# Kernel tuning notes

Hardware: AMD Instinct MI355X
Metric: run time of the kernel (lower is better)

The kernel has to match this reference:

```python
import jax, jax.numpy as jnp
import numpy as np

N_NODES = 25000
N_EDGES = 400000
N_GRAPHS = 1000
HID = 185
IN_CH = 9
EPS = 1e-5  # BatchNorm eps (eval mode: uses running stats)


def setup_inputs() -> dict:
    key = jax.random.key(0)
    ks = jax.random.split(key, 12)
    x = jax.random.normal(ks[0], (N_NODES, IN_CH), jnp.float32)
    edge_index = jax.random.randint(ks[1], (2, N_EDGES), 0, N_NODES, jnp.int32)
    batch = jnp.sort(jax.random.randint(ks[2], (N_NODES,), 0, N_GRAPHS, jnp.int32))
    W0 = jax.random.normal(ks[3], (IN_CH, HID), jnp.float32) * 0.3
    b0 = jnp.zeros((HID,), jnp.float32)
    W_h = jax.random.normal(ks[4], (3, HID, HID), jnp.float32) * 0.07
    b_h = jnp.zeros((3, HID), jnp.float32)
    bn_gamma = 1.0 + 0.1 * jax.random.normal(ks[5], (4, HID), jnp.float32)
    bn_beta = 0.1 * jax.random.normal(ks[6], (4, HID), jnp.float32)
    bn_mean = 0.1 * jax.random.normal(ks[7], (4, HID), jnp.float32)
    bn_var = jax.random.uniform(ks[8], (4, HID), jnp.float32, 0.5, 1.5)
    W_jk = jax.random.normal(ks[9], (4 * HID, HID), jnp.float32) * 0.05
    b_jk = jnp.zeros((HID,), jnp.float32)
    W_out = jax.random.normal(ks[10], (HID, 1), jnp.float32) * 0.1
    b_out = jnp.zeros((1,), jnp.float32)
    return dict(x=x, edge_index=edge_index, batch=batch, W0=W0, b0=b0,
                W_h=W_h, b_h=b_h, bn_gamma=bn_gamma, bn_beta=bn_beta,
                bn_mean=bn_mean, bn_var=bn_var, W_jk=W_jk, b_jk=b_jk,
                W_out=W_out, b_out=b_out)


def reference(x, edge_index, batch, W0, b0, W_h, b_h, bn_gamma, bn_beta,
              bn_mean, bn_var, W_jk, b_jk, W_out, b_out):
    N = x.shape[0]
    # GCN normalization with self-loops (gcn_norm, edge_weight = 1)
    loop = jnp.arange(N, dtype=edge_index.dtype)
    src = jnp.concatenate([edge_index[0], loop])  # [E+N]
    dst = jnp.concatenate([edge_index[1], loop])  # [E+N]
    deg = jax.ops.segment_sum(jnp.ones_like(dst, dtype=x.dtype), dst, num_segments=N)
    dis = jnp.where(deg > 0, jax.lax.rsqrt(jnp.maximum(deg, 1.0)), 0.0)
    enorm = dis[src] * dis[dst]  # [E+N]

    def gcn_conv(h, W, b):
        h = h @ W                                   # [N, HID]
        msg = h[src] * enorm[:, None]               # gather + scale, [E+N, HID]
        return jax.ops.segment_sum(msg, dst, num_segments=N) + b

    def bn_relu(h, i):
        h = (h - bn_mean[i]) * jax.lax.rsqrt(bn_var[i] + EPS) * bn_gamma[i] + bn_beta[i]
        return jax.nn.relu(h)  # dropout is identity in eval mode

    xs = []
    h = bn_relu(gcn_conv(x, W0, b0), 0)
    xs.append(h)
    for i in range(3):
        h = bn_relu(gcn_conv(h, W_h[i], b_h[i]), i + 1)
        xs.append(h)
    # JumpingKnowledge 'cat' + internal lin (740 -> 185)
    h = jnp.concatenate(xs, axis=-1) @ W_jk + b_jk  # [N, HID]
    # global_max_pool over graphs
    pooled = jax.ops.segment_max(h, batch, num_segments=N_GRAPHS)  # [G, HID]
    return pooled @ W_out + b_out  # [G, 1]
```

## Files before the change

kernel.cpp:

```cpp
#include <hip/hip_runtime.h>
#include <hip/hip_bf16.h>

#define N_NODES 25000
#define N_EDGES 400000
#define N_GRAPHS 1000
#define HID 185
#define EPS 1e-5f
#define XPITCH 768

typedef __attribute__((ext_vector_type(8))) short bf16x8;
typedef __attribute__((ext_vector_type(4))) float f32x4;

__device__ __forceinline__ short f2bf(float f) {
    union { float f; unsigned u; } v; v.f = f;
    unsigned r = v.u + 0x7FFFu + ((v.u >> 16) & 1u);
    return (short)(r >> 16);
}
__device__ __forceinline__ float bfl(unsigned u) { return __uint_as_float(u << 16); }
__device__ __forceinline__ float bfh(unsigned u) { return __uint_as_float(u & 0xFFFF0000u); }
__device__ __forceinline__ unsigned pk2(float lo, float hi) {
    return (unsigned)(unsigned short)f2bf(lo) | ((unsigned)(unsigned short)f2bf(hi) << 16);
}

#define GLD16(g, l) __builtin_amdgcn_global_load_lds( \
    (const __attribute__((address_space(1))) unsigned*)(const void*)(g), \
    (__attribute__((address_space(3))) unsigned*)(void*)(l), 16, 0, 0)

__global__ void k_init(int* cnt, int* cursor) {
    int i = blockIdx.x * blockDim.x + threadIdx.x;
    if (i < N_NODES) { cnt[i] = 0; cursor[i] = 0; }
}

__global__ void k_deg(const int* __restrict__ dst, int* cnt, int E) {
    int i = blockIdx.x * blockDim.x + threadIdx.x;
    if (i < E) atomicAdd(&cnt[dst[i]], 1);
}

__global__ __launch_bounds__(256) void k_scan_part(const int* __restrict__ cnt,
                                                   int* __restrict__ bsum,
                                                   float* __restrict__ dis, int N) {
    int i = blockIdx.x * 256 + threadIdx.x;
    int v = (i < N) ? cnt[i] : 0;
    if (i < N) dis[i] = rsqrtf((float)(v + 1));
    #pragma unroll
    for (int off = 32; off; off >>= 1) v += __shfl_down(v, off);
    __shared__ int s[4];
    if ((threadIdx.x & 63) == 0) s[threadIdx.x >> 6] = v;
    __syncthreads();
    if (threadIdx.x == 0) bsum[blockIdx.x] = s[0] + s[1] + s[2] + s[3];
}

__global__ __launch_bounds__(128) void k_scan_mid(const int* __restrict__ bsum,
                                                  int* __restrict__ boff, int NB) {
    __shared__ int s[128];
    int t = threadIdx.x;
    int v = (t < NB) ? bsum[t] : 0;
    s[t] = v; __syncthreads();
    for (int off = 1; off < 128; off <<= 1) {
        int x = (t >= off) ? s[t - off] : 0;
        __syncthreads();
        s[t] += x;
        __syncthreads();
    }
    if (t < NB) boff[t] = s[t] - v;
}

__global__ __launch_bounds__(256) void k_scan_add(const int* __restrict__ cnt,
                                                  const int* __restrict__ boff,
                                                  int* __restrict__ rowptr, int N) {
    __shared__ int s[256];
    int t = threadIdx.x;
    int i = blockIdx.x * 256 + t;
    int v = (i < N) ? cnt[i] : 0;
    s[t] = v; __syncthreads();
    for (int off = 1; off < 256; off <<= 1) {
        int x = (t >= off) ? s[t - off] : 0;
        __syncthreads();
        s[t] += x;
        __syncthreads();
    }
    if (i < N) rowptr[i + 1] = boff[blockIdx.x] + s[t];
    if (i == 0) rowptr[0] = 0;
}

__global__ void k_scatter(const int* __restrict__ src, const int* __restrict__ dst,
                          const float* __restrict__ dis, const int* __restrict__ rowptr,
                          int* cursor, int* __restrict__ csr_src,
                          float* __restrict__ csr_w, int E) {
    int e = blockIdx.x * blockDim.x + threadIdx.x;
    if (e < E) {
        int d = dst[e];
        int s = src[e];
        int pos = atomicAdd(&cursor[d], 1);
        int o = rowptr[d] + pos;
        csr_src[o] = s;
        csr_w[o] = dis[s];
    }
}

__global__ void k_prep_w(const float* __restrict__ W_h, const float* __restrict__ W_jk,
                         const float* __restrict__ b0, const float* __restrict__ b_h,
                         const float* __restrict__ gamma, const float* __restrict__ beta,
                         const float* __restrict__ mean, const float* __restrict__ var,
                         short* __restrict__ Wt_h, short* __restrict__ Wt_jk,
                         float* __restrict__ bnsc, float* __restrict__ bnsh) {
    int idx = blockIdx.x * 256 + threadIdx.x;
    const int HW = 3 * 192 * 192;
    const int JW = 192 * 768;
    if (idx < HW) {
        int l = idx / (192 * 192);
        int r = idx % (192 * 192);
        int n = r / 192, k = r % 192;
        float v = (n < HID && k < HID) ? W_h[(l * HID + k) * HID + n] : 0.0f;
        Wt_h[idx] = f2bf(v);
    } else if (idx < HW + JW) {
        int j2 = idx - HW;
        int n = j2 / 768, kk = j2 % 768;
        int l = kk / 192, j = kk % 192;
        float v = (n < HID && j < HID) ? W_jk[(l * HID + j) * HID + n] : 0.0f;
        Wt_jk[j2] = f2bf(v);
    } else if (idx < HW + JW + 4 * 192) {
        int li = idx - HW - JW;
        int l = li / 192, c = li % 192;
        float sc = 0.0f, sh = 0.0f;
        if (c < HID) {
            float bb = (l == 0) ? b0[c] : b_h[(l - 1) * HID + c];
            sc = rsqrtf(var[l * HID + c] + EPS) * gamma[l * HID + c];
            sh = (bb - mean[l * HID + c]) * sc + beta[l * HID + c];
        }
        bnsc[li] = sc;
        bnsh[li] = sh;
    }
}

__global__ void k_aggr0(const float* __restrict__ x, const float* __restrict__ dis,
                        const int* __restrict__ rowptr, const int* __restrict__ csr_src,
                        const float* __restrict__ csr_w, float* __restrict__ xa, int N) {
    int idx = blockIdx.x * blockDim.x + threadIdx.x;
    int n = idx >> 4;
    int c = idx & 15;
    if (n >= N || c >= 9) return;
    float dn = dis[n];
    float acc = x[n * 9 + c] * dn;
    int e = rowptr[n], end = rowptr[n + 1];
    for (; e + 4 <= end; e += 4) {
        int s0 = csr_src[e], s1 = csr_src[e + 1], s2 = csr_src[e + 2], s3 = csr_src[e + 3];
        float w0 = csr_w[e], w1 = csr_w[e + 1], w2 = csr_w[e + 2], w3 = csr_w[e + 3];
        float v0 = x[s0 * 9 + c], v1 = x[s1 * 9 + c], v2 = x[s2 * 9 + c], v3 = x[s3 * 9 + c];
        acc += v0 * w0 + v1 * w1 + v2 * w2 + v3 * w3;
    }
    for (; e < end; ++e)
        acc += x[csr_src[e] * 9 + c] * csr_w[e];
    xa[n * 9 + c] = acc * dn;
}

__global__ __launch_bounds__(192) void k_gemm0(const float* __restrict__ A,
                                               const float* __restrict__ W,
                                               const float* __restrict__ bnsc,
                                               const float* __restrict__ bnsh,
                                               short* __restrict__ xcat, int N) {
    __shared__ float As[8 * 9];
    const int tid = threadIdx.x;
    const int r0 = blockIdx.x * 8;
    for (int idx = tid; idx < 72; idx += 192) {
        int r = idx & 7, k = idx >> 3;
        int row = r0 + r;
        As[idx] = (row < N) ? A[row * 9 + k] : 0.0f;
    }
    __syncthreads();
    const int c = tid;
    float res[8];
    #pragma unroll
    for (int r = 0; r < 8; ++r) res[r] = 0.0f;
    if (c < HID) {
        float acc[8] = {0,0,0,0,0,0,0,0};
        for (int k = 0; k < 9; ++k) {
            float w = W[k * HID + c];
            #pragma unroll
            for (int r = 0; r < 8; ++r) acc[r] += As[k * 8 + r] * w;
        }
        float sc = bnsc[c], sh = bnsh[c];
        #pragma unroll
        for (int r = 0; r < 8; ++r)
            res[r] = fmaxf(acc[r] * sc + sh, 0.0f);
    }
    #pragma unroll
    for (int r = 0; r < 8; ++r) {
        int row = r0 + r;
        if (row < N) xcat[row * XPITCH + c] = (c < HID) ? f2bf(res[r]) : (short)0;
    }
}

template<int KCH>
__global__ __launch_bounds__(256, 3) void k_mgemm(const short* __restrict__ A,
                                                  const short* __restrict__ Bt,
                                                  short* __restrict__ Cout, int N) {
    __shared__ short As[2][64 * 32];
    const int tid = threadIdx.x;
    const int wave = tid >> 6;
    const int lane = tid & 63;
    const int quad = lane >> 4;
    const int lm = lane & 15;
    const int r0 = blockIdx.x * 64;
    const int KTOT = KCH * 32;
    const int srow = tid >> 2;
    const int sseg = (tid & 3) ^ ((srow >> 1) & 3);
    const long gbase = (long)(r0 + srow) * XPITCH + sseg * 8;
    const int axor = (lm >> 1) & 3;

    f32x4 acc[4][3];
    #pragma unroll
    for (int i = 0; i < 4; ++i)
        #pragma unroll
        for (int j = 0; j < 3; ++j) acc[i][j] = (f32x4){0.f, 0.f, 0.f, 0.f};

    GLD16(A + gbase, &As[0][tid * 8]);

    #pragma unroll
    for (int g = 0; g < KCH / 6; ++g) {
        bf16x8 b[3][6];
        #pragma unroll
        for (int j = 0; j < 6; ++j)
            #pragma unroll
            for (int nt = 0; nt < 3; ++nt)
                b[nt][j] = *(const bf16x8*)(Bt + (wave * 48 + nt * 16 + lm) * KTOT
                                            + (g * 6 + j) * 32 + quad * 8);
        #pragma unroll
        for (int j = 0; j < 6; ++j) {
            const int kc = g * 6 + j;
            __syncthreads();
            if (kc + 1 < KCH)
                GLD16(A + gbase + (kc + 1) * 32, &As[(kc + 1) & 1][tid * 8]);
            bf16x8 a[4];
            #pragma unroll
            for (int mt = 0; mt < 4; ++mt)
                a[mt] = *(const bf16x8*)(&As[kc & 1][(mt * 16 + lm) * 32 + (quad ^ axor) * 8]);
            #pragma unroll
            for (int mt = 0; mt < 4; ++mt)
                #pragma unroll
                for (int nt = 0; nt < 3; ++nt)
                    acc[mt][nt] = __builtin_amdgcn_mfma_f32_16x16x32_bf16(
                        a[mt], b[nt][j], acc[mt][nt], 0, 0, 0);
        }
    }
    #pragma unroll
    for (int mt = 0; mt < 4; ++mt) {
        #pragma unroll
        for (int nt = 0; nt < 3; ++nt) {
            int col = wave * 48 + nt * 16 + lm;
            #pragma unroll
            for (int r = 0; r < 4; ++r) {
                int row = r0 + mt * 16 + quad * 4 + r;
                if (row < N) Cout[row * 192 + col] = f2bf(acc[mt][nt][r]);
            }
        }
    }
}

__global__ __launch_bounds__(256) void k_aggr_bn(const short* __restrict__ tmp16,
                                                 const float* __restrict__ dis,
                                                 const int* __restrict__ rowptr,
                                                 const int* __restrict__ csr_src,
                                                 const float* __restrict__ csr_w,
                                                 const float* __restrict__ bnsc,
                                                 const float* __restrict__ bnsh,
                                                 short* __restrict__ outp, int N) {
    int n = (blockIdx.x << 2) + (threadIdx.x >> 6);
    if (n >= N) return;
    int lane = threadIdx.x & 63;
    int c0 = (lane < 48) ? (lane << 2) : 0;
    float dn = dis[n];
    float a0, a1, a2, a3;
    {
        uint2 v = *(const uint2*)(tmp16 + (size_t)n * 192 + c0);
        a0 = bfl(v.x) * dn; a1 = bfh(v.x) * dn; a2 = bfl(v.y) * dn; a3 = bfh(v.y) * dn;
    }
    int e = rowptr[n], end = rowptr[n + 1];
    for (; e + 4 <= end; e += 4) {
        int s0 = csr_src[e], s1 = csr_src[e + 1], s2 = csr_src[e + 2], s3 = csr_src[e + 3];
        float w0 = csr_w[e], w1 = csr_w[e + 1], w2 = csr_w[e + 2], w3 = csr_w[e + 3];
        uint2 v0 = *(const uint2*)(tmp16 + (size_t)s0 * 192 + c0);
        uint2 v1 = *(const uint2*)(tmp16 + (size_t)s1 * 192 + c0);
        uint2 v2 = *(const uint2*)(tmp16 + (size_t)s2 * 192 + c0);
        uint2 v3 = *(const uint2*)(tmp16 + (size_t)s3 * 192 + c0);
        a0 += bfl(v0.x) * w0; a1 += bfh(v0.x) * w0; a2 += bfl(v0.y) * w0; a3 += bfh(v0.y) * w0;
        a0 += bfl(v1.x) * w1; a1 += bfh(v1.x) * w1; a2 += bfl(v1.y) * w1; a3 += bfh(v1.y) * w1;
        a0 += bfl(v2.x) * w2; a1 += bfh(v2.x) * w2; a2 += bfl(v2.y) * w2; a3 += bfh(v2.y) * w2;
        a0 += bfl(v3.x) * w3; a1 += bfh(v3.x) * w3; a2 += bfl(v3.y) * w3; a3 += bfh(v3.y) * w3;
    }
    for (; e < end; ++e) {
        int s = csr_src[e];
        float w = csr_w[e];
        uint2 v = *(const uint2*)(tmp16 + (size_t)s * 192 + c0);
        a0 += bfl(v.x) * w; a1 += bfh(v.x) * w; a2 += bfl(v.y) * w; a3 += bfh(v.y) * w;
    }
    float4 sc = *(const float4*)(bnsc + c0);
    float4 sh = *(const float4*)(bnsh + c0);
    float o0 = fmaxf(a0 * dn * sc.x + sh.x, 0.0f);
    float o1 = fmaxf(a1 * dn * sc.y + sh.y, 0.0f);
    float o2 = fmaxf(a2 * dn * sc.z + sh.z, 0.0f);
    float o3 = fmaxf(a3 * dn * sc.w + sh.w, 0.0f);
    if (lane < 48) {
        uint2 p;
        p.x = pk2(o0, o1);
        p.y = pk2(o2, o3);
        *(uint2*)(outp + (size_t)n * XPITCH + c0) = p;
    }
}

__global__ __launch_bounds__(192) void k_pool_out(const short* __restrict__ jk,
                                                  const int* __restrict__ batch,
                                                  const float* __restrict__ b_jk,
                                                  const float* __restrict__ W_out,
                                                  const float* __restrict__ b_out,
                                                  float* __restrict__ out, int N) {
    __shared__ int bounds[2];
    __shared__ float partial[3];
    const int g = blockIdx.x;
    const int tid = threadIdx.x;
    if (tid < 2) {
        int key = g + tid;
        int lo = 0, hi = N;
        while (lo < hi) {
            int mid = (lo + hi) >> 1;
            if (batch[mid] < key) lo = mid + 1; else hi = mid;
        }
        bounds[tid] = lo;
    }
    __syncthreads();
    const int beg = bounds[0], end = bounds[1];
    float mx = -3.4e38f;
    for (int n = beg; n < end; ++n)
        mx = fmaxf(mx, bfl((unsigned)(unsigned short)jk[(size_t)n * 192 + tid]));
    float p = (tid < HID) ? (mx + b_jk[tid]) * W_out[tid] : 0.0f;
    #pragma unroll
    for (int off = 32; off; off >>= 1) p += __shfl_down(p, off);
    if ((tid & 63) == 0) partial[tid >> 6] = p;
    __syncthreads();
    if (tid == 0) out[g] = partial[0] + partial[1] + partial[2] + b_out[0];
}

extern "C" void kernel_launch(void* const* d_in, const int* in_sizes, int n_in,
                              void* d_out, int out_size, void* d_ws, size_t ws_size,
                              hipStream_t stream) {
    const float* x      = (const float*)d_in[0];
    const int*   ei     = (const int*)  d_in[1];
    const int*   batch  = (const int*)  d_in[2];
    const float* W0     = (const float*)d_in[3];
    const float* b0     = (const float*)d_in[4];
    const float* W_h    = (const float*)d_in[5];
    const float* b_h    = (const float*)d_in[6];
    const float* gamma  = (const float*)d_in[7];
    const float* beta   = (const float*)d_in[8];
    const float* mean   = (const float*)d_in[9];
    const float* var    = (const float*)d_in[10];
    const float* W_jk   = (const float*)d_in[11];
    const float* b_jk   = (const float*)d_in[12];
    const float* W_out  = (const float*)d_in[13];
    const float* b_out  = (const float*)d_in[14];
    float* out = (float*)d_out;

    const int N = N_NODES, E = N_EDGES, G = N_GRAPHS, H = HID;
    const int NB = (N + 255) / 256;

    float* dis   = (float*)d_ws;
    float* xa    = dis + 25024;
    float* csr_w = xa + 225024;
    float* bnsc  = csr_w + 400000;
    float* bnsh  = bnsc + 768;
    short* xcat  = (short*)(bnsh + 768);
    short* tmp16 = xcat + 19200000;
    short* Wt_h  = tmp16 + 4800000;
    short* Wt_jk = Wt_h + 110592;
    int* rowptr  = (int*)(Wt_jk + 147456);
    int* cnt     = rowptr + 25024;
    int* cursor  = cnt + 25024;
    int* csr_src = cursor + 25024;
    int* bsum    = csr_src + 400000;
    int* boff    = bsum + 128;

    const int* src = ei;
    const int* dst = ei + E;

    k_init<<<NB, 256, 0, stream>>>(cnt, cursor);
    k_deg<<<(E + 255) / 256, 256, 0, stream>>>(dst, cnt, E);
    k_scan_part<<<NB, 256, 0, stream>>>(cnt, bsum, dis, N);
    k_scan_mid<<<1, 128, 0, stream>>>(bsum, boff, NB);
    k_scan_add<<<NB, 256, 0, stream>>>(cnt, boff, rowptr, N);
    k_scatter<<<(E + 255) / 256, 256, 0, stream>>>(src, dst, dis, rowptr, cursor,
                                                   csr_src, csr_w, E);
    k_prep_w<<<(3 * 192 * 192 + 192 * 768 + 4 * 192 + 255) / 256, 256, 0, stream>>>(
        W_h, W_jk, b0, b_h, gamma, beta, mean, var, Wt_h, Wt_jk, bnsc, bnsh);

    k_aggr0<<<(N * 16 + 255) / 256, 256, 0, stream>>>(x, dis, rowptr, csr_src, csr_w, xa, N);
    k_gemm0<<<(N + 7) / 8, 192, 0, stream>>>(xa, W0, bnsc, bnsh, xcat, N);

    const int MB = (N + 63) / 64;
    for (int l = 1; l < 4; ++l) {
        k_mgemm<6><<<MB, 256, 0, stream>>>(xcat + (l - 1) * 192,
                                           Wt_h + (l - 1) * 192 * 192, tmp16, N);
        k_aggr_bn<<<(N + 3) / 4, 256, 0, stream>>>(tmp16, dis, rowptr, csr_src, csr_w,
                                                   bnsc + l * 192, bnsh + l * 192,
                                                   xcat + l * 192, N);
    }

    k_mgemm<24><<<MB, 256, 0, stream>>>(xcat, Wt_jk, tmp16, N);

    k_pool_out<<<G, 192, 0, stream>>>(tmp16, batch, b_jk, W_out, b_out, out, N);
}
```

Before: 317.3 us.

## Cut launches: merge setup, fold scan, fuse layer-0 aggregation into GEMM, drop LDS staging

Merges the count-zeroing and weight-prep kernels into one, removes the mid-scan kernel by having each block reduce preceding block sums itself, and reuses rowptr as the scatter cursor, which turns rowptr into end offsets. Layer-0 aggregation is fused into the small input GEMM, so the xa intermediate disappears. The MFMA GEMM loses its LDS double-buffered async loads and its occupancy hint, and now reads A and B fragments straight from global memory. This trades fewer launches and less LDS synchronization for GEMM loads that may be less efficient and more redundant.

```diff
diff --git a/kernel.cpp b/kernel.cpp
--- a/kernel.cpp
+++ b/kernel.cpp
@@ -22,13 +22,43 @@
     return (unsigned)(unsigned short)f2bf(lo) | ((unsigned)(unsigned short)f2bf(hi) << 16);
 }
 
-#define GLD16(g, l) __builtin_amdgcn_global_load_lds( \
-    (const __attribute__((address_space(1))) unsigned*)(const void*)(g), \
-    (__attribute__((address_space(3))) unsigned*)(void*)(l), 16, 0, 0)
-
-__global__ void k_init(int* cnt, int* cursor) {
-    int i = blockIdx.x * blockDim.x + threadIdx.x;
-    if (i < N_NODES) { cnt[i] = 0; cursor[i] = 0; }
+#define HW (3 * 192 * 192)
+#define JW (192 * 768)
+#define CNTPAD 25024
+__global__ void k_setup(const float* __restrict__ W_h, const float* __restrict__ W_jk,
+                        const float* __restrict__ b0, const float* __restrict__ b_h,
+                        const float* __restrict__ gamma, const float* __restrict__ beta,
+                        const float* __restrict__ mean, const float* __restrict__ var,
+                        int* __restrict__ cnt,
+                        short* __restrict__ Wt_h, short* __restrict__ Wt_jk,
+                        float* __restrict__ bnsc, float* __restrict__ bnsh) {
+    int idx = blockIdx.x * 256 + threadIdx.x;
+    if (idx < CNTPAD) { cnt[idx] = 0; return; }
+    int p = idx - CNTPAD;
+    if (p < HW) {
+        int l = p / (192 * 192);
+        int r = p % (192 * 192);
+        int n = r / 192, k = r % 192;
+        float v = (n < HID && k < HID) ? W_h[(l * HID + k) * HID + n] : 0.0f;
+        Wt_h[p] = f2bf(v);
+    } else if (p < HW + JW) {
+        int j2 = p - HW;
+        int n = j2 / 768, kk = j2 % 768;
+        int l = kk / 192, j = kk % 192;
+        float v = (n < HID && j < HID) ? W_jk[(l * HID + j) * HID + n] : 0.0f;
+        Wt_jk[j2] = f2bf(v);
+    } else if (p < HW + JW + 4 * 192) {
+        int li = p - HW - JW;
+        int l = li / 192, c = li % 192;
+        float sc = 0.0f, sh = 0.0f;
+        if (c < HID) {
+            float bb = (l == 0) ? b0[c] : b_h[(l - 1) * HID + c];
+            sc = rsqrtf(var[l * HID + c] + EPS) * gamma[l * HID + c];
+            sh = (bb - mean[l * HID + c]) * sc + beta[l * HID + c];
+        }
+        bnsc[li] = sc;
+        bnsh[li] = sh;
+    }
 }
 
 __global__ void k_deg(const int* __restrict__ dst, int* cnt, int E) {
@@ -50,122 +80,78 @@
     if (threadIdx.x == 0) bsum[blockIdx.x] = s[0] + s[1] + s[2] + s[3];
 }
 
-__global__ __launch_bounds__(128) void k_scan_mid(const int* __restrict__ bsum,
-                                                  int* __restrict__ boff, int NB) {
-    __shared__ int s[128];
-    int t = threadIdx.x;
-    int v = (t < NB) ? bsum[t] : 0;
-    s[t] = v; __syncthreads();
-    for (int off = 1; off < 128; off <<= 1) {
-        int x = (t >= off) ? s[t - off] : 0;
-        __syncthreads();
-        s[t] += x;
-        __syncthreads();
-    }
-    if (t < NB) boff[t] = s[t] - v;
-}
-
 __global__ __launch_bounds__(256) void k_scan_add(const int* __restrict__ cnt,
-                                                  const int* __restrict__ boff,
+                                                  const int* __restrict__ bsum,
                                                   int* __restrict__ rowptr, int N) {
     __shared__ int s[256];
-    int t = threadIdx.x;
-    int i = blockIdx.x * 256 + t;
+    const int t = threadIdx.x;
+    const int b = blockIdx.x;
+    int partial = 0;
+    for (int i = t; i < b; i += 256) partial += bsum[i];
+    s[t] = partial; __syncthreads();
+    for (int off = 128; off; off >>= 1) {
+        if (t < off) s[t] += s[t + off];
+        __syncthreads();
+    }
+    const int base = s[0];
+    __syncthreads();
+    int i = b * 256 + t;
     int v = (i < N) ? cnt[i] : 0;
     s[t] = v; __syncthreads();
     for (int off = 1; off < 256; off <<= 1) {
-        int x = (t >= off) ? s[t - off] : 0;
+        int x2 = (t >= off) ? s[t - off] : 0;
         __syncthreads();
-        s[t] += x;
+        s[t] += x2;
         __syncthreads();
     }
-    if (i < N) rowptr[i + 1] = boff[blockIdx.x] + s[t];
-    if (i == 0) rowptr[0] = 0;
+    if (i < N) rowptr[i] = base + s[t] - v;
 }
 
 __global__ void k_scatter(const int* __restrict__ src, const int* __restrict__ dst,
-                          const float* __restrict__ dis, const int* __restrict__ rowptr,
-                          int* cursor, int* __restrict__ csr_src,
+                          const float* __restrict__ dis,
+                          int* rowptr, int* __restrict__ csr_src,
                           float* __restrict__ csr_w, int E) {
     int e = blockIdx.x * blockDim.x + threadIdx.x;
     if (e < E) {
         int d = dst[e];
         int s = src[e];
-        int pos = atomicAdd(&cursor[d], 1);
-        int o = rowptr[d] + pos;
+        int o = atomicAdd(&rowptr[d], 1);
         csr_src[o] = s;
         csr_w[o] = dis[s];
     }
 }
 
-__global__ void k_prep_w(const float* __restrict__ W_h, const float* __restrict__ W_jk,
-                         const float* __restrict__ b0, const float* __restrict__ b_h,
-                         const float* __restrict__ gamma, const float* __restrict__ beta,
-                         const float* __restrict__ mean, const float* __restrict__ var,
-                         short* __restrict__ Wt_h, short* __restrict__ Wt_jk,
-                         float* __restrict__ bnsc, float* __restrict__ bnsh) {
-    int idx = blockIdx.x * 256 + threadIdx.x;
-    const int HW = 3 * 192 * 192;
-    const int JW = 192 * 768;
-    if (idx < HW) {
-        int l = idx / (192 * 192);
-        int r = idx % (192 * 192);
-        int n = r / 192, k = r % 192;
-        float v = (n < HID && k < HID) ? W_h[(l * HID + k) * HID + n] : 0.0f;
-        Wt_h[idx] = f2bf(v);
-    } else if (idx < HW + JW) {
-        int j2 = idx - HW;
-        int n = j2 / 768, kk = j2 % 768;
-        int l = kk / 192, j = kk % 192;
-        float v = (n < HID && j < HID) ? W_jk[(l * HID + j) * HID + n] : 0.0f;
-        Wt_jk[j2] = f2bf(v);
-    } else if (idx < HW + JW + 4 * 192) {
-        int li = idx - HW - JW;
-        int l = li / 192, c = li % 192;
-        float sc = 0.0f, sh = 0.0f;
-        if (c < HID) {
-            float bb = (l == 0) ? b0[c] : b_h[(l - 1) * HID + c];
-            sc = rsqrtf(var[l * HID + c] + EPS) * gamma[l * HID + c];
-            sh = (bb - mean[l * HID + c]) * sc + beta[l * HID + c];
-        }
-        bnsc[li] = sc;
-        bnsh[li] = sh;
-    }
-}
-
-__global__ void k_aggr0(const float* __restrict__ x, const float* __restrict__ dis,
-                        const int* __restrict__ rowptr, const int* __restrict__ csr_src,
-                        const float* __restrict__ csr_w, float* __restrict__ xa, int N) {
-    int idx = blockIdx.x * blockDim.x + threadIdx.x;
-    int n = idx >> 4;
-    int c = idx & 15;
-    if (n >= N || c >= 9) return;
-    float dn = dis[n];
-    float acc = x[n * 9 + c] * dn;
-    int e = rowptr[n], end = rowptr[n + 1];
-    for (; e + 4 <= end; e += 4) {
-        int s0 = csr_src[e], s1 = csr_src[e + 1], s2 = csr_src[e + 2], s3 = csr_src[e + 3];
-        float w0 = csr_w[e], w1 = csr_w[e + 1], w2 = csr_w[e + 2], w3 = csr_w[e + 3];
-        float v0 = x[s0 * 9 + c], v1 = x[s1 * 9 + c], v2 = x[s2 * 9 + c], v3 = x[s3 * 9 + c];
-        acc += v0 * w0 + v1 * w1 + v2 * w2 + v3 * w3;
-    }
-    for (; e < end; ++e)
-        acc += x[csr_src[e] * 9 + c] * csr_w[e];
-    xa[n * 9 + c] = acc * dn;
-}
-
-__global__ __launch_bounds__(192) void k_gemm0(const float* __restrict__ A,
-                                               const float* __restrict__ W,
-                                               const float* __restrict__ bnsc,
-                                               const float* __restrict__ bnsh,
-                                               short* __restrict__ xcat, int N) {
-    __shared__ float As[8 * 9];
+__global__ __launch_bounds__(192) void k_gemm0f(const float* __restrict__ x,
+                                                const float* __restrict__ dis,
+                                                const int* __restrict__ rowptr,
+                                                const int* __restrict__ csr_src,
+                                                const float* __restrict__ csr_w,
+                                                const float* __restrict__ W,
+                                                const float* __restrict__ bnsc,
+                                                const float* __restrict__ bnsh,
+                                                short* __restrict__ xcat, int N) {
+    __shared__ float As[72];
     const int tid = threadIdx.x;
     const int r0 = blockIdx.x * 8;
-    for (int idx = tid; idx < 72; idx += 192) {
-        int r = idx & 7, k = idx >> 3;
+    if (tid < 72) {
+        int r = tid & 7, k = tid >> 3;
         int row = r0 + r;
-        As[idx] = (row < N) ? A[row * 9 + k] : 0.0f;
+        float val = 0.0f;
+        if (row < N && k < 9) {
+            float dn = dis[row];
+            float acc = x[row * 9 + k] * dn;
+            int end = rowptr[row];
+            int e = row ? rowptr[row - 1] : 0;
+            for (; e + 4 <= end; e += 4) {
+                int s0 = csr_src[e], s1 = csr_src[e+1], s2 = csr_src[e+2], s3 = csr_src[e+3];
+                float w0 = csr_w[e], w1 = csr_w[e+1], w2 = csr_w[e+2], w3 = csr_w[e+3];
+                acc += x[s0*9+k]*w0 + x[s1*9+k]*w1 + x[s2*9+k]*w2 + x[s3*9+k]*w3;
+            }
+            for (; e < end; ++e)
+                acc += x[csr_src[e] * 9 + k] * csr_w[e];
+            val = acc * dn;
+        }
+        As[tid] = val;
     }
     __syncthreads();
     const int c = tid;
@@ -192,10 +178,9 @@
 }
 
 template<int KCH>
-__global__ __launch_bounds__(256, 3) void k_mgemm(const short* __restrict__ A,
-                                                  const short* __restrict__ Bt,
-                                                  short* __restrict__ Cout, int N) {
-    __shared__ short As[2][64 * 32];
+__global__ __launch_bounds__(256) void k_mgemm(const short* __restrict__ A,
+                                               const short* __restrict__ Bt,
+                                               short* __restrict__ Cout, int N) {
     const int tid = threadIdx.x;
     const int wave = tid >> 6;
     const int lane = tid & 63;
@@ -203,10 +188,8 @@
     const int lm = lane & 15;
     const int r0 = blockIdx.x * 64;
     const int KTOT = KCH * 32;
-    const int srow = tid >> 2;
-    const int sseg = (tid & 3) ^ ((srow >> 1) & 3);
-    const long gbase = (long)(r0 + srow) * XPITCH + sseg * 8;
-    const int axor = (lm >> 1) & 3;
+    const short* Ab = A + (size_t)(r0 + lm) * XPITCH + quad * 8;
+    const short* Bb = Bt + (size_t)(wave * 48 + lm) * KTOT + quad * 8;
 
     f32x4 acc[4][3];
     #pragma unroll
@@ -214,33 +197,22 @@
         #pragma unroll
         for (int j = 0; j < 3; ++j) acc[i][j] = (f32x4){0.f, 0.f, 0.f, 0.f};
 
-    GLD16(A + gbase, &As[0][tid * 8]);
-
-    #pragma unroll
     for (int g = 0; g < KCH / 6; ++g) {
-        bf16x8 b[3][6];
-        #pragma unroll
-        for (int j = 0; j < 6; ++j)
-            #pragma unroll
-            for (int nt = 0; nt < 3; ++nt)
-                b[nt][j] = *(const bf16x8*)(Bt + (wave * 48 + nt * 16 + lm) * KTOT
-                                            + (g * 6 + j) * 32 + quad * 8);
         #pragma unroll
         for (int j = 0; j < 6; ++j) {
             const int kc = g * 6 + j;
-            __syncthreads();
-            if (kc + 1 < KCH)
-                GLD16(A + gbase + (kc + 1) * 32, &As[(kc + 1) & 1][tid * 8]);
-            bf16x8 a[4];
+            bf16x8 b[3];
             #pragma unroll
-            for (int mt = 0; mt < 4; ++mt)
-                a[mt] = *(const bf16x8*)(&As[kc & 1][(mt * 16 + lm) * 32 + (quad ^ axor) * 8]);
+            for (int nt = 0; nt < 3; ++nt)
+                b[nt] = *(const bf16x8*)(Bb + (size_t)nt * 16 * KTOT + kc * 32);
             #pragma unroll
-            for (int mt = 0; mt < 4; ++mt)
+            for (int mt = 0; mt < 4; ++mt) {
+                bf16x8 a = *(const bf16x8*)(Ab + (size_t)mt * 16 * XPITCH + kc * 32);
                 #pragma unroll
                 for (int nt = 0; nt < 3; ++nt)
                     acc[mt][nt] = __builtin_amdgcn_mfma_f32_16x16x32_bf16(
-                        a[mt], b[nt][j], acc[mt][nt], 0, 0, 0);
+                        a, b[nt], acc[mt][nt], 0, 0, 0);
+            }
         }
     }
     #pragma unroll
@@ -275,7 +247,8 @@
         uint2 v = *(const uint2*)(tmp16 + (size_t)n * 192 + c0);
         a0 = bfl(v.x) * dn; a1 = bfh(v.x) * dn; a2 = bfl(v.y) * dn; a3 = bfh(v.y) * dn;
     }
-    int e = rowptr[n], end = rowptr[n + 1];
+    int end = rowptr[n];
+    int e = n ? rowptr[n - 1] : 0;
     for (; e + 4 <= end; e += 4) {
         int s0 = csr_src[e], s1 = csr_src[e + 1], s2 = csr_src[e + 2], s3 = csr_src[e + 3];
         float w0 = csr_w[e], w1 = csr_w[e + 1], w2 = csr_w[e + 2], w3 = csr_w[e + 3];
@@ -360,12 +333,11 @@
     const float* b_out  = (const float*)d_in[14];
     float* out = (float*)d_out;
 
-    const int N = N_NODES, E = N_EDGES, G = N_GRAPHS, H = HID;
+    const int N = N_NODES, E = N_EDGES, G = N_GRAPHS;
     const int NB = (N + 255) / 256;
 
     float* dis   = (float*)d_ws;
-    float* xa    = dis + 25024;
-    float* csr_w = xa + 225024;
+    float* csr_w = dis + 25024;
     float* bnsc  = csr_w + 400000;
     float* bnsh  = bnsc + 768;
     short* xcat  = (short*)(bnsh + 768);
@@ -374,26 +346,21 @@
     short* Wt_jk = Wt_h + 110592;
     int* rowptr  = (int*)(Wt_jk + 147456);
     int* cnt     = rowptr + 25024;
-    int* cursor  = cnt + 25024;
-    int* csr_src = cursor + 25024;
+    int* csr_src = cnt + 25024;
     int* bsum    = csr_src + 400000;
-    int* boff    = bsum + 128;
 
     const int* src = ei;
     const int* dst = ei + E;
 
-    k_init<<<NB, 256, 0, stream>>>(cnt, cursor);
+    k_setup<<<(CNTPAD + HW + JW + 4 * 192 + 255) / 256, 256, 0, stream>>>(
+        W_h, W_jk, b0, b_h, gamma, beta, mean, var, cnt, Wt_h, Wt_jk, bnsc, bnsh);
     k_deg<<<(E + 255) / 256, 256, 0, stream>>>(dst, cnt, E);
     k_scan_part<<<NB, 256, 0, stream>>>(cnt, bsum, dis, N);
-    k_scan_mid<<<1, 128, 0, stream>>>(bsum, boff, NB);
-    k_scan_add<<<NB, 256, 0, stream>>>(cnt, boff, rowptr, N);
-    k_scatter<<<(E + 255) / 256, 256, 0, stream>>>(src, dst, dis, rowptr, cursor,
-                                                   csr_src, csr_w, E);
-    k_prep_w<<<(3 * 192 * 192 + 192 * 768 + 4 * 192 + 255) / 256, 256, 0, stream>>>(
-        W_h, W_jk, b0, b_h, gamma, beta, mean, var, Wt_h, Wt_jk, bnsc, bnsh);
-
-    k_aggr0<<<(N * 16 + 255) / 256, 256, 0, stream>>>(x, dis, rowptr, csr_src, csr_w, xa, N);
-    k_gemm0<<<(N + 7) / 8, 192, 0, stream>>>(xa, W0, bnsc, bnsh, xcat, N);
+    k_scan_add<<<NB, 256, 0, stream>>>(cnt, bsum, rowptr, N);
+    k_scatter<<<(E + 255) / 256, 256, 0, stream>>>(src, dst, dis, rowptr, csr_src, csr_w, E);
+
+    k_gemm0f<<<(N + 7) / 8, 192, 0, stream>>>(x, dis, rowptr, csr_src, csr_w,
+                                              W0, bnsc, bnsh, xcat, N);
 
     const int MB = (N + 63) / 64;
     for (int l = 1; l < 4; ++l) {
```

Result: slower. 339.0 us (+6.8%).
